# Kernel tuning notes

Hardware: AMD Instinct MI355X
Metric: run time of the kernel (lower is better)

The kernel has to match this reference:

```python
import jax, jax.numpy as jnp
import numpy as np

N_STEPS = 128
B = 32768
H = 64
T0, T1 = 0.0, 1.0
L = 1.0
DT = (T1 - T0) / N_STEPS

# ---- synthesized Equation methods (shapes match the torch forward) ----
def U_fn(x):            return jnp.sum(x * x, axis=-1, keepdims=True)            # [.., B, 1]
def D_fn(n):            return 0.5 + 0.1 * jnp.abs(n)                            # [B, 1] > 0
def alpha_fn(n):        return 0.5 * (n + 1.0)
def beta_fn(n):         return 0.4 * jnp.abs(n) + 0.1
def sigma0_fn(x):       # [B,3,3]
    return 0.5 * jnp.eye(3, dtype=x.dtype) + 0.1 * x[..., :, None] * x[..., None, :]
def T_inv_fn(x):        # [B,3,3]
    nrm = 1.0 + jnp.sum(x * x, axis=-1)[..., None, None]
    return jnp.eye(3, dtype=x.dtype) - x[..., :, None] * x[..., None, :] / nrm
def f_fn(t, n, x, p, y, z):  # y complex [B,1], z complex [B,3]
    return p * y + 0.1 * (1.0 + t) * jnp.sum(z, axis=-1, keepdims=True)
def g_fn(n, x):
    return jnp.sum(x, axis=-1, keepdims=True).astype(jnp.complex64)

def mlp_c(W1, b1, W2, b2, inp):
    """MLP with complex output via paired real/imag heads."""
    h = jnp.tanh(inp @ W1 + b1)
    o = h @ W2 + b2
    d = o.shape[-1] // 2
    return (o[..., :d] + 1j * o[..., d:]).astype(jnp.complex64)

def feat(n, x, p):
    return jnp.concatenate([n, x, p], axis=-1)  # [B, 5]


def setup_inputs() -> dict:
    key = jax.random.key(0)
    ks = jax.random.split(key, 16)
    # polar sample -> 3D start point on the sphere (tran_2to3)
    theta = jax.random.uniform(ks[0], (B, 1)) * jnp.pi
    phi = jax.random.uniform(ks[1], (B, 1)) * 2.0 * jnp.pi
    x0 = jnp.concatenate([jnp.sin(theta) * jnp.cos(phi),
                          jnp.sin(theta) * jnp.sin(phi),
                          jnp.cos(theta)], axis=-1)                       # [B,3]
    # Brownian increments and paths (get_position)
    delta_B = jnp.sqrt(DT) * jax.random.normal(ks[2], (N_STEPS, B, 3), jnp.float32)
    process_X = jnp.concatenate([x0[None], x0[None] + jnp.cumsum(delta_B, 0)], 0)  # [N+1,B,3]
    # birth-death jump counting process
    dN = (jax.random.randint(ks[3], (N_STEPS, B, 1), 0, 3) - 1).astype(jnp.float32)
    n0 = jnp.full((1, B, 1), 10.0, jnp.float32)
    process_N = jnp.concatenate([n0, n0 + jnp.cumsum(dN, 0)], 0)           # [N+1,B,1]
    discrete_p = jax.random.uniform(ks[4], (N_STEPS + 1, B, 1), jnp.float32)
    discrete_t = jnp.linspace(T0, T1, N_STEPS + 1, dtype=jnp.float32)

    def w(k, shape, fan_in):
        return jax.random.normal(k, shape, jnp.float32) / np.sqrt(fan_in)
    inp = dict(process_N=process_N, process_X=process_X, discrete_p=discrete_p,
               discrete_t=discrete_t, delta_B=delta_B,
               Wr1=w(ks[5], (5, H), 5), br1=jnp.zeros((H,)),
               Wr2=w(ks[6], (H, 2), H), br2=jnp.zeros((2,)),
               Wg1=w(ks[7], (N_STEPS, 5, H), 5), bg1=jnp.zeros((N_STEPS, H)),
               Wg2=w(ks[8], (N_STEPS, H, 6), H), bg2=jnp.zeros((N_STEPS, 6)),
               Wj1=w(ks[9], (N_STEPS, 5, H), 5), bj1=jnp.zeros((N_STEPS, H)),
               Wj2=w(ks[10], (N_STEPS, H, 2), H), bj2=jnp.zeros((N_STEPS, 2)))
    return inp


def bsde_forward(process_N, process_X, discrete_p, discrete_t, delta_B,
                 Wr1, br1, Wr2, br2, Wg1, bg1, Wg2, bg2, Wj1, bj1, Wj2, bj2):
    # functional bookkeeping: exp(-cumsum(roll(1j*p*U(x),1) with [0]=0) * dt)
    functional = 1j * discrete_p * U_fn(process_X)                         # [N+1,B,1] c64
    functional = jnp.concatenate([jnp.zeros_like(functional[:1]), functional[:-1]], 0)
    exp_functional = jnp.exp(-jnp.cumsum(functional, axis=0) * DT)         # [N+1,B,1] c64

    u0 = mlp_c(Wr1, br1, Wr2, br2, feat(process_N[0], process_X[0], discrete_p[0]))  # [B,1]
    delta_N_all = jnp.round(process_N[1:] - process_N[:-1])                # [N,B,1]

    xs = (process_N[:-1], process_X[:-1], discrete_p[:-1], discrete_t[:-1],
          delta_B, exp_functional[:-1], delta_N_all,
          Wg1, bg1, Wg2, bg2, Wj1, bj1, Wj2, bj2)

    def step(u, xi):
        (n, x, p, t, dB, ef, dNi, wg1, bg1_, wg2, bg2_, wj1, bj1_, wj2, bj2_) = xi
        ft = feat(n, x, p)
        grad_u = mlp_c(wg1, bg1_, wg2, bg2_, ft)                           # [B,3] c64
        S = sigma0_fn(x)                                                   # [B,3,3]
        Ti = T_inv_fn(x)                                                   # [B,3,3]
        k = jnp.sqrt(2.0 * D_fn(n)) / L                                    # [B,1]
        kg = k * grad_u                                                    # [B,3] c64
        M = jnp.einsum('bij,bkj->bik', Ti, S).astype(jnp.complex64)        # T_inv @ sigma^T
        grad_bmm = jnp.einsum('bi,bij,bj->b', kg, M,
                              dB.astype(jnp.complex64))[:, None]           # [B,1] c64
        ui  = mlp_c(wj1, bj1_, wj2, bj2_, ft)
        uip = mlp_c(wj1, bj1_, wj2, bj2_, feat(n + 1.0, x, p))
        uim = mlp_c(wj1, bj1_, wj2, bj2_, feat(n - 1.0, x, p))
        dup, dum = uip - ui, uim - ui
        fv = f_fn(t, n, x, p, u / ef, grad_u)
        delt = grad_bmm - (alpha_fn(n) * dup + beta_fn(n) * dum) * DT - fv * DT
        delt = jnp.where(dNi > 0, dup, jnp.where(dNi < 0, dum, delt))
        return u + ef * delt, None

    u, _ = jax.lax.scan(step, u0, xs)
    g = exp_functional[-1] * g_fn(process_N[-1], process_X[-1])
    return u, g


def reference(process_N, process_X, discrete_p, discrete_t, delta_B,
              Wr1, br1, Wr2, br2, Wg1, bg1, Wg2, bg2, Wj1, bj1, Wj2, bj2):
    return bsde_forward(process_N, process_X, discrete_p, discrete_t, delta_B,
                        Wr1, br1, Wr2, br2, Wg1, bg1, Wg2, bg2, Wj1, bj1, Wj2, bj2)
```

## Files before the change

kernel.cpp:

```cpp
#include <hip/hip_runtime.h>
#include <math.h>

#define NSTEPS 128
#define BATCH  32768
#define HID    64
#define BLK    512

constexpr float DTf = 1.0f / 128.0f;
constexpr float TWO_LOG2E = 2.88539008177792681f;

typedef float v2f __attribute__((ext_vector_type(2)));

__device__ __forceinline__ v2f v2ld(const float* p) { return *(const v2f*)p; }
__device__ __forceinline__ v2f bc(float s) { v2f r = {s, s}; return r; }
__device__ __forceinline__ v2f pkfma(v2f a, v2f b, v2f c) {
    return __builtin_elementwise_fma(a, b, c);
}

struct CD { float c, dre, dim; };

__device__ __forceinline__ float fast_tanh(float x) {
    float e = __builtin_amdgcn_exp2f(x * TWO_LOG2E);
    return 1.0f - 2.0f * __builtin_amdgcn_rcpf(e + 1.0f);
}
__device__ __forceinline__ v2f fast_tanh2(v2f z) {
    v2f zs = z * TWO_LOG2E;
    v2f e;
    e.x = __builtin_amdgcn_exp2f(zs.x);
    e.y = __builtin_amdgcn_exp2f(zs.y);
    v2f e1 = e + 1.0f;
    v2f r;
    r.x = __builtin_amdgcn_rcpf(e1.x);
    r.y = __builtin_amdgcn_rcpf(e1.y);
    return pkfma(bc(-2.0f), r, bc(1.0f));
}

__device__ __forceinline__ void grad_mlp(
    float n, float x0, float x1, float x2, float p,
    const float* __restrict__ w1, const float* __restrict__ b1,
    const float* __restrict__ w2, const float* __restrict__ b2,
    float& og0, float& og1, float& og2, float& og3, float& og4, float& og5)
{
    v2f og01 = { b2[0], b2[1] };
    v2f og23 = { b2[2], b2[3] };
    v2f og45 = { b2[4], b2[5] };
#pragma unroll 4
    for (int j = 0; j < HID; j += 2) {
        v2f z = pkfma(bc(n),  v2ld(w1 + j),
                pkfma(bc(x0), v2ld(w1 + HID   + j),
                pkfma(bc(x1), v2ld(w1 + 2*HID + j),
                pkfma(bc(x2), v2ld(w1 + 3*HID + j),
                pkfma(bc(p),  v2ld(w1 + 4*HID + j), v2ld(b1 + j))))));
        v2f h = fast_tanh2(z);
        const float* wj = w2 + j*6;
        og01 = pkfma(bc(h.x), v2ld(wj),     pkfma(bc(h.y), v2ld(wj + 6),  og01));
        og23 = pkfma(bc(h.x), v2ld(wj + 2), pkfma(bc(h.y), v2ld(wj + 8),  og23));
        og45 = pkfma(bc(h.x), v2ld(wj + 4), pkfma(bc(h.y), v2ld(wj + 10), og45));
    }
    og0 = og01.x; og1 = og01.y; og2 = og23.x;
    og3 = og23.y; og4 = og45.x; og5 = og45.y;
}

template<bool USE_TD>
__device__ __forceinline__ void jump_mlp(
    float n, float x0, float x1, float x2, float p,
    const float* __restrict__ v1, const float* __restrict__ c1,
    const float* __restrict__ vw2, const float* __restrict__ Td,
    float& dup0, float& dup1, float& dum0, float& dum1)
{
    v2f dup01 = { 0.f, 0.f };
    v2f dum01 = { 0.f, 0.f };
#pragma unroll 4
    for (int j = 0; j < HID; j += 2) {
        v2f d  = v2ld(v1 + j);
        v2f zb = pkfma(bc(n), d,
                 pkfma(bc(x0), v2ld(v1 + HID   + j),
                 pkfma(bc(x1), v2ld(v1 + 2*HID + j),
                 pkfma(bc(x2), v2ld(v1 + 3*HID + j),
                 pkfma(bc(p),  v2ld(v1 + 4*HID + j), v2ld(c1 + j))))));
        v2f T  = fast_tanh2(zb);
        v2f Tv;
        if (USE_TD) Tv = v2ld(Td + j);
        else { Tv.x = fast_tanh(d.x); Tv.y = fast_tanh(d.y); }
        v2f a    = T * Tv;
        v2f oma2 = pkfma(-a, a, bc(1.0f));
        v2f r;
        r.x = __builtin_amdgcn_rcpf(oma2.x);
        r.y = __builtin_amdgcn_rcpf(oma2.y);
        v2f s1 = (T + Tv) * r;
        v2f u1 = s1 - T;
        v2f ep = pkfma(-s1, a, u1);
        v2f s2 = (T - Tv) * r;
        v2f u2 = s2 - T;
        v2f em = pkfma(s2, a, u2);
        v2f wv0 = v2ld(vw2 + 2*j);
        v2f wv1 = v2ld(vw2 + 2*j + 2);
        dup01 = pkfma(bc(ep.x), wv0, pkfma(bc(ep.y), wv1, dup01));
        dum01 = pkfma(bc(em.x), wv0, pkfma(bc(em.y), wv1, dum01));
    }
    dup0 = dup01.x; dup1 = dup01.y;
    dum0 = dum01.x; dum1 = dum01.y;
}

__device__ __forceinline__ void jump_mlp_1s(
    float n, float x0, float x1, float x2, float p, float sgn,
    const float* __restrict__ v1, const float* __restrict__ c1,
    const float* __restrict__ vw2, const float* __restrict__ Td,
    float& e0, float& e1)
{
    v2f acc = { 0.f, 0.f };
#pragma unroll 4
    for (int j = 0; j < HID; j += 2) {
        v2f d  = v2ld(v1 + j);
        v2f zb = pkfma(bc(n), d,
                 pkfma(bc(x0), v2ld(v1 + HID   + j),
                 pkfma(bc(x1), v2ld(v1 + 2*HID + j),
                 pkfma(bc(x2), v2ld(v1 + 3*HID + j),
                 pkfma(bc(p),  v2ld(v1 + 4*HID + j), v2ld(c1 + j))))));
        v2f T   = fast_tanh2(zb);
        v2f Tsv = bc(sgn) * v2ld(Td + j);
        v2f as  = T * Tsv;
        v2f oma = pkfma(-as, as, bc(1.0f));
        v2f r;
        r.x = __builtin_amdgcn_rcpf(oma.x);
        r.y = __builtin_amdgcn_rcpf(oma.y);
        v2f s1 = (T + Tsv) * r;
        v2f u1 = s1 - T;
        v2f e  = pkfma(-s1, as, u1);
        acc = pkfma(bc(e.x), v2ld(vw2 + 2*j), pkfma(bc(e.y), v2ld(vw2 + 2*j + 2), acc));
    }
    e0 = acc.x; e1 = acc.y;
}

template<bool USE_TD>
__device__ __forceinline__ CD step_core(
    float n, float x0, float x1, float x2, float p, float t,
    float db0, float db1, float db2, float dN, float phi,
    const float* __restrict__ w1, const float* __restrict__ b1,
    const float* __restrict__ w2, const float* __restrict__ b2,
    const float* __restrict__ v1, const float* __restrict__ c1,
    const float* __restrict__ vw2, const float* __restrict__ Td)
{
    float og0, og1, og2, og3, og4, og5;
    grad_mlp(n,x0,x1,x2,p, w1,b1,w2,b2, og0,og1,og2,og3,og4,og5);
    float dup0, dup1, dum0, dum1;
    jump_mlp<USE_TD>(n,x0,x1,x2,p, v1,c1,vw2,Td, dup0,dup1,dum0,dum1);

    float r2    = fmaf(x0,x0, fmaf(x1,x1, x2*x2));
    float gamma = 0.1f - (0.5f + 0.1f*r2) * __builtin_amdgcn_rcpf(1.0f + r2);
    float xdb   = fmaf(x0,db0, fmaf(x1,db1, x2*db2));
    float kc    = sqrtf(fmaf(0.2f, fabsf(n), 1.0f));
    float gdb_r = fmaf(og0,db0, fmaf(og1,db1, og2*db2));
    float gdb_i = fmaf(og3,db0, fmaf(og4,db1, og5*db2));
    float gx_r  = fmaf(og0,x0,  fmaf(og1,x1,  og2*x2));
    float gx_i  = fmaf(og3,x0,  fmaf(og4,x1,  og5*x2));
    float gb_r  = kc * fmaf(gamma*xdb, gx_r, 0.5f*gdb_r);
    float gb_i  = kc * fmaf(gamma*xdb, gx_i, 0.5f*gdb_i);

    float alpha = 0.5f*(n + 1.0f);
    float beta  = fmaf(0.4f, fabsf(n), 0.1f);
    float cf    = 0.1f*(1.0f + t)*DTf;
    float d0r = gb_r - (alpha*dup0 + beta*dum0)*DTf - cf*(og0+og1+og2);
    float d0i = gb_i - (alpha*dup1 + beta*dum1)*DTf - cf*(og3+og4+og5);

    float c, sr, si;
    if (dN > 0.5f)       { c = 1.0f;          sr = dup0; si = dup1; }
    else if (dN < -0.5f) { c = 1.0f;          sr = dum0; si = dum1; }
    else                 { c = 1.0f - p*DTf;  sr = d0r;  si = d0i;  }

    float sp, cp;
    __sincosf(phi, &sp, &cp);
    CD o;
    o.c   = c;
    o.dre = fmaf(cp, sr,  sp*si);
    o.dim = fmaf(cp, si, -sp*sr);
    return o;
}

__device__ __forceinline__ void mlp_u0(
    float n, float x0, float x1, float x2, float p,
    const float* __restrict__ w1, const float* __restrict__ b1,
    const float* __restrict__ w2, const float* __restrict__ b2,
    float& ur, float& ui)
{
    v2f o01 = { b2[0], b2[1] };
#pragma unroll 4
    for (int j = 0; j < HID; j += 2) {
        v2f z = pkfma(bc(n),  v2ld(w1 + j),
                pkfma(bc(x0), v2ld(w1 + HID   + j),
                pkfma(bc(x1), v2ld(w1 + 2*HID + j),
                pkfma(bc(x2), v2ld(w1 + 3*HID + j),
                pkfma(bc(p),  v2ld(w1 + 4*HID + j), v2ld(b1 + j))))));
        v2f h = fast_tanh2(z);
        o01 = pkfma(bc(h.x), v2ld(w2 + 2*j), pkfma(bc(h.y), v2ld(w2 + 2*j + 2), o01));
    }
    ur = o01.x; ui = o01.y;
}

__global__ void __launch_bounds__(256) k_phi(
    const float* __restrict__ X, const float* __restrict__ P,
    float* __restrict__ phi, float* __restrict__ phiF)
{
    int b = blockIdx.x*256 + threadIdx.x;
    double s = 0.0;
    for (int k = 0; k < NSTEPS; k++) {
        size_t idx = (size_t)k*BATCH + b;
        phi[idx] = (float)(DTf * s);
        float p = P[idx];
        const float* xp = X + idx*3;
        float x0 = xp[0], x1 = xp[1], x2 = xp[2];
        s += (double)p * (double)(x0*x0 + x1*x1 + x2*x2);
    }
    phiF[b] = (float)(DTf * s);
}

__global__ void __launch_bounds__(BLK) k_step(
    const float* __restrict__ N,  const float* __restrict__ X,
    const float* __restrict__ P,  const float* __restrict__ Tarr,
    const float* __restrict__ dB,
    const float* __restrict__ Wg1, const float* __restrict__ bg1,
    const float* __restrict__ Wg2, const float* __restrict__ bg2,
    const float* __restrict__ Wj1, const float* __restrict__ bj1,
    const float* __restrict__ Wj2, const float* __restrict__ bj2,
    const float* __restrict__ phiA, float* __restrict__ cA, float2* __restrict__ dA)
{
    int k = blockIdx.y;
    const float* w1  = Wg1 + k*5*HID;
    const float* b1  = bg1 + k*HID;
    const float* w2  = Wg2 + k*HID*6;
    const float* b2  = bg2 + k*6;
    const float* v1  = Wj1 + k*5*HID;
    const float* c1  = bj1 + k*HID;
    const float* vw2 = Wj2 + k*HID*2;
    float t = Tarr[k];

    __shared__ float Td[HID];
    __shared__ unsigned short sorig[BLK];
    __shared__ int cnt[2];
    if (threadIdx.x < HID) Td[threadIdx.x] = fast_tanh(v1[threadIdx.x]);
    if (threadIdx.x == 0) { cnt[0] = 0; cnt[1] = 0; }
    __syncthreads();

    int tid  = threadIdx.x;
    int base = blockIdx.x*BLK;
    {
        size_t i0 = (size_t)k*BATCH + base + tid;
        float n0  = N[i0];
        float dN0 = N[i0 + BATCH] - n0;
        bool full0 = (dN0 == 0.0f);
        int pos = full0 ? atomicAdd(&cnt[0], 1) : (BLK-1) - atomicAdd(&cnt[1], 1);
        sorig[pos] = (unsigned short)tid;
    }
    __syncthreads();

    int ob = base + sorig[tid];
    size_t idx = (size_t)k*BATCH + ob;
    float n  = N[idx], p = P[idx];
    float dN = N[idx + BATCH] - n;
    const float* xp  = X  + idx*3;
    const float* dbp = dB + idx*3;
    float x0 = xp[0],  x1 = xp[1],  x2 = xp[2];
    float db0 = dbp[0], db1 = dbp[1], db2 = dbp[2];
    float phi = phiA[idx];
    bool  g   = (dN == 0.0f);

    float c, sr, si;
    if (__ballot(g) != 0ull) {
        float dup0, dup1, dum0, dum1;
        jump_mlp<true>(n,x0,x1,x2,p, v1,c1,vw2,Td, dup0,dup1,dum0,dum1);
        float og0, og1, og2, og3, og4, og5;
        grad_mlp(n,x0,x1,x2,p, w1,b1,w2,b2, og0,og1,og2,og3,og4,og5);

        float r2    = fmaf(x0,x0, fmaf(x1,x1, x2*x2));
        float gamma = 0.1f - (0.5f + 0.1f*r2) * __builtin_amdgcn_rcpf(1.0f + r2);
        float xdb   = fmaf(x0,db0, fmaf(x1,db1, x2*db2));
        float kc    = sqrtf(fmaf(0.2f, fabsf(n), 1.0f));
        float gdb_r = fmaf(og0,db0, fmaf(og1,db1, og2*db2));
        float gdb_i = fmaf(og3,db0, fmaf(og4,db1, og5*db2));
        float gx_r  = fmaf(og0,x0,  fmaf(og1,x1,  og2*x2));
        float gx_i  = fmaf(og3,x0,  fmaf(og4,x1,  og5*x2));
        float gb_r  = kc * fmaf(gamma*xdb, gx_r, 0.5f*gdb_r);
        float gb_i  = kc * fmaf(gamma*xdb, gx_i, 0.5f*gdb_i);

        float alpha = 0.5f*(n + 1.0f);
        float beta  = fmaf(0.4f, fabsf(n), 0.1f);
        float cf    = 0.1f*(1.0f + t)*DTf;
        float d0r = gb_r - (alpha*dup0 + beta*dum0)*DTf - cf*(og0+og1+og2);
        float d0i = gb_i - (alpha*dup1 + beta*dum1)*DTf - cf*(og3+og4+og5);

        if (dN > 0.5f)       { c = 1.0f;          sr = dup0; si = dup1; }
        else if (dN < -0.5f) { c = 1.0f;          sr = dum0; si = dum1; }
        else                 { c = 1.0f - p*DTf;  sr = d0r;  si = d0i;  }
    } else {
        jump_mlp_1s(n,x0,x1,x2,p, dN, v1,c1,vw2,Td, sr, si);
        c = 1.0f;
    }

    float sp, cp;
    __sincosf(phi, &sp, &cp);
    size_t oidx = (size_t)k*BATCH + ob;
    cA[oidx] = c;
    dA[oidx] = make_float2(fmaf(cp, sr,  sp*si), fmaf(cp, si, -sp*sr));
}

__global__ void __launch_bounds__(256) k_combine(
    const float* __restrict__ N, const float* __restrict__ X, const float* __restrict__ P,
    const float* __restrict__ Wr1, const float* __restrict__ br1,
    const float* __restrict__ Wr2, const float* __restrict__ br2,
    const float* __restrict__ cA, const float2* __restrict__ dA,
    const float* __restrict__ phiF, float* __restrict__ out, int full)
{
    int b = blockIdx.x*256 + threadIdx.x;
    const float* xp = X + (size_t)b*3;
    float ur, ui;
    mlp_u0(N[b], xp[0], xp[1], xp[2], P[b], Wr1, br1, Wr2, br2, ur, ui);
#pragma unroll 8
    for (int k = 0; k < NSTEPS; k++) {
        size_t idx = (size_t)k*BATCH + b;
        float  c = cA[idx];
        float2 d = dA[idx];
        ur = fmaf(c, ur, d.x);
        ui = fmaf(c, ui, d.y);
    }
    float phi = phiF[b];
    const float* xf = X + ((size_t)NSTEPS*BATCH + b)*3;
    float s = xf[0] + xf[1] + xf[2];
    float sp, cp;
    __sincosf(phi, &sp, &cp);
    float gre =  s*cp;
    float gim = -s*sp;
    if (full) {
        out[b]           = ur;
        out[BATCH + b]   = ui;
        out[2*BATCH + b] = gre;
        out[3*BATCH + b] = gim;
    } else {
        out[b]         = ur;
        out[BATCH + b] = gre;
    }
}

__global__ void __launch_bounds__(256) k_fused(
    const float* __restrict__ N,  const float* __restrict__ X,
    const float* __restrict__ P,  const float* __restrict__ Tarr,
    const float* __restrict__ dB,
    const float* __restrict__ Wr1, const float* __restrict__ br1,
    const float* __restrict__ Wr2, const float* __restrict__ br2,
    const float* __restrict__ Wg1, const float* __restrict__ bg1,
    const float* __restrict__ Wg2, const float* __restrict__ bg2,
    const float* __restrict__ Wj1, const float* __restrict__ bj1,
    const float* __restrict__ Wj2, const float* __restrict__ bj2,
    float* __restrict__ out, int full)
{
    int b = blockIdx.x*256 + threadIdx.x;
    float ur, ui;
    {
        const float* xp = X + (size_t)b*3;
        mlp_u0(N[b], xp[0], xp[1], xp[2], P[b], Wr1, br1, Wr2, br2, ur, ui);
    }
    double s = 0.0;
    for (int k = 0; k < NSTEPS; k++) {
        size_t idx = (size_t)k*BATCH + b;
        float n = N[idx], p = P[idx], t = Tarr[k];
        const float* xp  = X  + idx*3;
        const float* dbp = dB + idx*3;
        float dN  = N[idx + BATCH] - n;
        float phi = (float)(DTf * s);
        CD cd = step_core<false>(n, xp[0], xp[1], xp[2], p, t,
                                 dbp[0], dbp[1], dbp[2], dN, phi,
                                 Wg1 + k*5*HID, bg1 + k*HID,
                                 Wg2 + k*HID*6, bg2 + k*6,
                                 Wj1 + k*5*HID, bj1 + k*HID,
                                 Wj2 + k*HID*2, nullptr);
        ur = fmaf(cd.c, ur, cd.dre);
        ui = fmaf(cd.c, ui, cd.dim);
        float x0 = xp[0], x1 = xp[1], x2 = xp[2];
        s += (double)p * (double)(x0*x0 + x1*x1 + x2*x2);
    }
    float phi = (float)(DTf * s);
    const float* xf = X + ((size_t)NSTEPS*BATCH + b)*3;
    float sm = xf[0] + xf[1] + xf[2];
    float sp, cp;
    __sincosf(phi, &sp, &cp);
    float gre =  sm*cp;
    float gim = -sm*sp;
    if (full) {
        out[b]           = ur;
        out[BATCH + b]   = ui;
        out[2*BATCH + b] = gre;
        out[3*BATCH + b] = gim;
    } else {
        out[b]         = ur;
        out[BATCH + b] = gre;
    }
}

extern "C" void kernel_launch(void* const* d_in, const int* in_sizes, int n_in,
                              void* d_out, int out_size, void* d_ws, size_t ws_size,
                              hipStream_t stream)
{
    const float* N    = (const float*)d_in[0];
    const float* X    = (const float*)d_in[1];
    const float* P    = (const float*)d_in[2];
    const float* Tarr = (const float*)d_in[3];
    const float* dB   = (const float*)d_in[4];
    const float* Wr1  = (const float*)d_in[5];
    const float* br1  = (const float*)d_in[6];
    const float* Wr2  = (const float*)d_in[7];
    const float* br2  = (const float*)d_in[8];
    const float* Wg1  = (const float*)d_in[9];
    const float* bg1  = (const float*)d_in[10];
    const float* Wg2  = (const float*)d_in[11];
    const float* bg2  = (const float*)d_in[12];
    const float* Wj1  = (const float*)d_in[13];
    const float* bj1  = (const float*)d_in[14];
    const float* Wj2  = (const float*)d_in[15];
    const float* bj2  = (const float*)d_in[16];
    float* out = (float*)d_out;

    const int full = (out_size >= 4*BATCH) ? 1 : 0;

    const size_t phi_elems = (size_t)NSTEPS*BATCH;
    const size_t need = (phi_elems + BATCH + phi_elems)*sizeof(float)
                      + phi_elems*sizeof(float2);

    if (ws_size >= need) {
        float*  phiA = (float*)d_ws;
        float*  phiF = phiA + phi_elems;
        float*  cA   = phiF + BATCH;
        float2* dA   = (float2*)(cA + phi_elems);

        k_phi<<<dim3(BATCH/256), dim3(256), 0, stream>>>(X, P, phiA, phiF);
        k_step<<<dim3(BATCH/BLK, NSTEPS), dim3(BLK), 0, stream>>>(
            N, X, P, Tarr, dB, Wg1, bg1, Wg2, bg2, Wj1, bj1, Wj2, bj2,
            phiA, cA, dA);
        k_combine<<<dim3(BATCH/256), dim3(256), 0, stream>>>(
            N, X, P, Wr1, br1, Wr2, br2, cA, dA, phiF, out, full);
    } else {
        k_fused<<<dim3(BATCH/256), dim3(256), 0, stream>>>(
            N, X, P, Tarr, dB, Wr1, br1, Wr2, br2,
            Wg1, bg1, Wg2, bg2, Wj1, bj1, Wj2, bj2, out, full);
    }
}
```

Measured before the change: 215.3 us.

## Compact full and jump samples globally into separate lists and specialized kernels

Adds a classify kernel that builds global per-step index lists of no-jump and jump samples, then launches separate kernels for each class so every wavefront runs only one code path. Before, samples were only sorted within each block, so mixed wavefronts still ran both paths. The cA array is dropped and the decay coefficient is recomputed from N and P in the combine loop, which cuts one write stream. This adds two kernel launches, a memset and an extra list write and read, and the gathered indices make memory access scattered.

```diff
diff --git a/kernel.cpp b/kernel.cpp
--- a/kernel.cpp
+++ b/kernel.cpp
@@ -4,7 +4,6 @@
 #define NSTEPS 128
 #define BATCH  32768
 #define HID    64
-#define BLK    512
 
 constexpr float DTf = 1.0f / 128.0f;
 constexpr float TWO_LOG2E = 2.88539008177792681f;
@@ -214,7 +213,40 @@
     phiF[b] = (float)(DTf * s);
 }
 
-__global__ void __launch_bounds__(BLK) k_step(
+__global__ void __launch_bounds__(256) k_classify(
+    const float* __restrict__ N,
+    unsigned short* __restrict__ fullList, unsigned short* __restrict__ jumpList,
+    int2* __restrict__ counters)
+{
+    int k   = blockIdx.y;
+    int tid = threadIdx.x;
+    int b   = blockIdx.x*256 + tid;
+
+    __shared__ int cnt[2];
+    __shared__ int gbase[2];
+    __shared__ unsigned short lf[256], lj[256];
+    if (tid == 0) { cnt[0] = 0; cnt[1] = 0; }
+    __syncthreads();
+
+    size_t i0 = (size_t)k*BATCH + b;
+    float n0  = N[i0];
+    float dN  = N[i0 + BATCH] - n0;
+    if (dN == 0.0f) {
+        int r = atomicAdd(&cnt[0], 1);
+        lf[r] = (unsigned short)b;
+    } else {
+        int r = atomicAdd(&cnt[1], 1);
+        lj[r] = (unsigned short)(b | (dN < 0.0f ? 0x8000 : 0));
+    }
+    __syncthreads();
+    if (tid == 0) gbase[0] = atomicAdd(&counters[k].x, cnt[0]);
+    if (tid == 1) gbase[1] = atomicAdd(&counters[k].y, cnt[1]);
+    __syncthreads();
+    if (tid < cnt[0]) fullList[(size_t)k*BATCH + gbase[0] + tid] = lf[tid];
+    if (tid < cnt[1]) jumpList[(size_t)k*BATCH + gbase[1] + tid] = lj[tid];
+}
+
+__global__ void __launch_bounds__(256) k_step_full(
     const float* __restrict__ N,  const float* __restrict__ X,
     const float* __restrict__ P,  const float* __restrict__ Tarr,
     const float* __restrict__ dB,
@@ -222,9 +254,15 @@
     const float* __restrict__ Wg2, const float* __restrict__ bg2,
     const float* __restrict__ Wj1, const float* __restrict__ bj1,
     const float* __restrict__ Wj2, const float* __restrict__ bj2,
-    const float* __restrict__ phiA, float* __restrict__ cA, float2* __restrict__ dA)
+    const float* __restrict__ phiA,
+    const unsigned short* __restrict__ fullList, const int2* __restrict__ counters,
+    float2* __restrict__ dA)
 {
     int k = blockIdx.y;
+    int count = counters[k].x;
+    int start = blockIdx.x*256;
+    if (start >= count) return;
+
     const float* w1  = Wg1 + k*5*HID;
     const float* b1  = bg1 + k*HID;
     const float* w2  = Wg2 + k*HID*6;
@@ -235,92 +273,111 @@
     float t = Tarr[k];
 
     __shared__ float Td[HID];
-    __shared__ unsigned short sorig[BLK];
-    __shared__ int cnt[2];
     if (threadIdx.x < HID) Td[threadIdx.x] = fast_tanh(v1[threadIdx.x]);
-    if (threadIdx.x == 0) { cnt[0] = 0; cnt[1] = 0; }
     __syncthreads();
 
-    int tid  = threadIdx.x;
-    int base = blockIdx.x*BLK;
-    {
-        size_t i0 = (size_t)k*BATCH + base + tid;
-        float n0  = N[i0];
-        float dN0 = N[i0 + BATCH] - n0;
-        bool full0 = (dN0 == 0.0f);
-        int pos = full0 ? atomicAdd(&cnt[0], 1) : (BLK-1) - atomicAdd(&cnt[1], 1);
-        sorig[pos] = (unsigned short)tid;
-    }
-    __syncthreads();
-
-    int ob = base + sorig[tid];
+    int slot = start + threadIdx.x;
+    bool act = slot < count;
+    int ob   = fullList[(size_t)k*BATCH + (act ? slot : count - 1)];
     size_t idx = (size_t)k*BATCH + ob;
-    float n  = N[idx], p = P[idx];
-    float dN = N[idx + BATCH] - n;
+    float n = N[idx], p = P[idx];
     const float* xp  = X  + idx*3;
     const float* dbp = dB + idx*3;
     float x0 = xp[0],  x1 = xp[1],  x2 = xp[2];
     float db0 = dbp[0], db1 = dbp[1], db2 = dbp[2];
     float phi = phiA[idx];
-    bool  g   = (dN == 0.0f);
-
-    float c, sr, si;
-    if (__ballot(g) != 0ull) {
-        float dup0, dup1, dum0, dum1;
-        jump_mlp<true>(n,x0,x1,x2,p, v1,c1,vw2,Td, dup0,dup1,dum0,dum1);
-        float og0, og1, og2, og3, og4, og5;
-        grad_mlp(n,x0,x1,x2,p, w1,b1,w2,b2, og0,og1,og2,og3,og4,og5);
-
-        float r2    = fmaf(x0,x0, fmaf(x1,x1, x2*x2));
-        float gamma = 0.1f - (0.5f + 0.1f*r2) * __builtin_amdgcn_rcpf(1.0f + r2);
-        float xdb   = fmaf(x0,db0, fmaf(x1,db1, x2*db2));
-        float kc    = sqrtf(fmaf(0.2f, fabsf(n), 1.0f));
-        float gdb_r = fmaf(og0,db0, fmaf(og1,db1, og2*db2));
-        float gdb_i = fmaf(og3,db0, fmaf(og4,db1, og5*db2));
-        float gx_r  = fmaf(og0,x0,  fmaf(og1,x1,  og2*x2));
-        float gx_i  = fmaf(og3,x0,  fmaf(og4,x1,  og5*x2));
-        float gb_r  = kc * fmaf(gamma*xdb, gx_r, 0.5f*gdb_r);
-        float gb_i  = kc * fmaf(gamma*xdb, gx_i, 0.5f*gdb_i);
-
-        float alpha = 0.5f*(n + 1.0f);
-        float beta  = fmaf(0.4f, fabsf(n), 0.1f);
-        float cf    = 0.1f*(1.0f + t)*DTf;
-        float d0r = gb_r - (alpha*dup0 + beta*dum0)*DTf - cf*(og0+og1+og2);
-        float d0i = gb_i - (alpha*dup1 + beta*dum1)*DTf - cf*(og3+og4+og5);
-
-        if (dN > 0.5f)       { c = 1.0f;          sr = dup0; si = dup1; }
-        else if (dN < -0.5f) { c = 1.0f;          sr = dum0; si = dum1; }
-        else                 { c = 1.0f - p*DTf;  sr = d0r;  si = d0i;  }
-    } else {
-        jump_mlp_1s(n,x0,x1,x2,p, dN, v1,c1,vw2,Td, sr, si);
-        c = 1.0f;
-    }
+
+    float dup0, dup1, dum0, dum1;
+    jump_mlp<true>(n,x0,x1,x2,p, v1,c1,vw2,Td, dup0,dup1,dum0,dum1);
+    float og0, og1, og2, og3, og4, og5;
+    grad_mlp(n,x0,x1,x2,p, w1,b1,w2,b2, og0,og1,og2,og3,og4,og5);
+
+    float r2    = fmaf(x0,x0, fmaf(x1,x1, x2*x2));
+    float gamma = 0.1f - (0.5f + 0.1f*r2) * __builtin_amdgcn_rcpf(1.0f + r2);
+    float xdb   = fmaf(x0,db0, fmaf(x1,db1, x2*db2));
+    float kc    = sqrtf(fmaf(0.2f, fabsf(n), 1.0f));
+    float gdb_r = fmaf(og0,db0, fmaf(og1,db1, og2*db2));
+    float gdb_i = fmaf(og3,db0, fmaf(og4,db1, og5*db2));
+    float gx_r  = fmaf(og0,x0,  fmaf(og1,x1,  og2*x2));
+    float gx_i  = fmaf(og3,x0,  fmaf(og4,x1,  og5*x2));
+    float gb_r  = kc * fmaf(gamma*xdb, gx_r, 0.5f*gdb_r);
+    float gb_i  = kc * fmaf(gamma*xdb, gx_i, 0.5f*gdb_i);
+
+    float alpha = 0.5f*(n + 1.0f);
+    float beta  = fmaf(0.4f, fabsf(n), 0.1f);
+    float cf    = 0.1f*(1.0f + t)*DTf;
+    float sr = gb_r - (alpha*dup0 + beta*dum0)*DTf - cf*(og0+og1+og2);
+    float si = gb_i - (alpha*dup1 + beta*dum1)*DTf - cf*(og3+og4+og5);
 
     float sp, cp;
     __sincosf(phi, &sp, &cp);
-    size_t oidx = (size_t)k*BATCH + ob;
-    cA[oidx] = c;
-    dA[oidx] = make_float2(fmaf(cp, sr,  sp*si), fmaf(cp, si, -sp*sr));
+    if (act)
+        dA[idx] = make_float2(fmaf(cp, sr,  sp*si), fmaf(cp, si, -sp*sr));
+}
+
+__global__ void __launch_bounds__(256) k_step_jump(
+    const float* __restrict__ N,  const float* __restrict__ X,
+    const float* __restrict__ P,
+    const float* __restrict__ Wj1, const float* __restrict__ bj1,
+    const float* __restrict__ Wj2,
+    const float* __restrict__ phiA,
+    const unsigned short* __restrict__ jumpList, const int2* __restrict__ counters,
+    float2* __restrict__ dA)
+{
+    int k = blockIdx.y;
+    int count = counters[k].y;
+    int start = blockIdx.x*256;
+    if (start >= count) return;
+
+    const float* v1  = Wj1 + k*5*HID;
+    const float* c1  = bj1 + k*HID;
+    const float* vw2 = Wj2 + k*HID*2;
+
+    __shared__ float Td[HID];
+    if (threadIdx.x < HID) Td[threadIdx.x] = fast_tanh(v1[threadIdx.x]);
+    __syncthreads();
+
+    int slot = start + threadIdx.x;
+    bool act = slot < count;
+    unsigned short ent = jumpList[(size_t)k*BATCH + (act ? slot : count - 1)];
+    float sgn = (ent & 0x8000) ? -1.0f : 1.0f;
+    int   ob  = ent & 0x7FFF;
+    size_t idx = (size_t)k*BATCH + ob;
+    float n = N[idx], p = P[idx];
+    const float* xp = X + idx*3;
+    float x0 = xp[0], x1 = xp[1], x2 = xp[2];
+    float phi = phiA[idx];
+
+    float sr, si;
+    jump_mlp_1s(n,x0,x1,x2,p, sgn, v1,c1,vw2,Td, sr, si);
+
+    float sp, cp;
+    __sincosf(phi, &sp, &cp);
+    if (act)
+        dA[idx] = make_float2(fmaf(cp, sr,  sp*si), fmaf(cp, si, -sp*sr));
 }
 
 __global__ void __launch_bounds__(256) k_combine(
     const float* __restrict__ N, const float* __restrict__ X, const float* __restrict__ P,
     const float* __restrict__ Wr1, const float* __restrict__ br1,
     const float* __restrict__ Wr2, const float* __restrict__ br2,
-    const float* __restrict__ cA, const float2* __restrict__ dA,
+    const float2* __restrict__ dA,
     const float* __restrict__ phiF, float* __restrict__ out, int full)
 {
     int b = blockIdx.x*256 + threadIdx.x;
     const float* xp = X + (size_t)b*3;
     float ur, ui;
     mlp_u0(N[b], xp[0], xp[1], xp[2], P[b], Wr1, br1, Wr2, br2, ur, ui);
-#pragma unroll 8
+    float nprev = N[b];
+#pragma unroll 4
     for (int k = 0; k < NSTEPS; k++) {
         size_t idx = (size_t)k*BATCH + b;
-        float  c = cA[idx];
+        float nnext = N[idx + BATCH];
+        float c = (nnext == nprev) ? (1.0f - P[idx]*DTf) : 1.0f;
         float2 d = dA[idx];
         ur = fmaf(c, ur, d.x);
         ui = fmaf(c, ui, d.y);
+        nprev = nnext;
     }
     float phi = phiF[b];
     const float* xf = X + ((size_t)NSTEPS*BATCH + b)*3;
@@ -421,21 +478,32 @@
     const int full = (out_size >= 4*BATCH) ? 1 : 0;
 
     const size_t phi_elems = (size_t)NSTEPS*BATCH;
-    const size_t need = (phi_elems + BATCH + phi_elems)*sizeof(float)
-                      + phi_elems*sizeof(float2);
+    const size_t off_phiF = phi_elems*4;
+    const size_t off_dA   = off_phiF + (size_t)BATCH*4;
+    const size_t off_fl   = off_dA + phi_elems*8;
+    const size_t off_jl   = off_fl + phi_elems*2;
+    const size_t off_cnt  = off_jl + phi_elems*2;
+    const size_t need     = off_cnt + NSTEPS*sizeof(int2);
 
     if (ws_size >= need) {
-        float*  phiA = (float*)d_ws;
-        float*  phiF = phiA + phi_elems;
-        float*  cA   = phiF + BATCH;
-        float2* dA   = (float2*)(cA + phi_elems);
-
+        char* ws = (char*)d_ws;
+        float*          phiA = (float*)ws;
+        float*          phiF = (float*)(ws + off_phiF);
+        float2*         dA   = (float2*)(ws + off_dA);
+        unsigned short* fL   = (unsigned short*)(ws + off_fl);
+        unsigned short* jL   = (unsigned short*)(ws + off_jl);
+        int2*           cnts = (int2*)(ws + off_cnt);
+
+        hipMemsetAsync(cnts, 0, NSTEPS*sizeof(int2), stream);
         k_phi<<<dim3(BATCH/256), dim3(256), 0, stream>>>(X, P, phiA, phiF);
-        k_step<<<dim3(BATCH/BLK, NSTEPS), dim3(BLK), 0, stream>>>(
+        k_classify<<<dim3(BATCH/256, NSTEPS), dim3(256), 0, stream>>>(N, fL, jL, cnts);
+        k_step_full<<<dim3(BATCH/256, NSTEPS), dim3(256), 0, stream>>>(
             N, X, P, Tarr, dB, Wg1, bg1, Wg2, bg2, Wj1, bj1, Wj2, bj2,
-            phiA, cA, dA);
+            phiA, fL, cnts, dA);
+        k_step_jump<<<dim3(BATCH/256, NSTEPS), dim3(256), 0, stream>>>(
+            N, X, P, Wj1, bj1, Wj2, phiA, jL, cnts, dA);
         k_combine<<<dim3(BATCH/256), dim3(256), 0, stream>>>(
-            N, X, P, Wr1, br1, Wr2, br2, cA, dA, phiF, out, full);
+            N, X, P, Wr1, br1, Wr2, br2, dA, phiF, out, full);
     } else {
         k_fused<<<dim3(BATCH/256), dim3(256), 0, stream>>>(
             N, X, P, Tarr, dB, Wr1, br1, Wr2, br2,
```

Measured after the change: 463.0 us. +115.1%, slower.

## Process four batch elements per thread in k_step to reuse weight loads

Applied to the files above, without the earlier changes.

Each thread in k_step now handles four sorted batch elements instead of one. Blocks shrink to 256 threads but cover a window of 1024 elements. The MLP weight loads for each hidden unit pair are hoisted out of the per-element loop and shared across all four elements, which cuts scalar/LDS weight traffic and adds independent work for latency hiding. In exchange, register pressure rises, the grid has fewer blocks, and the coarser grouping can make the uniform-branch test (any full-step element in the wave) trigger the expensive path more often.

```diff
diff --git a/kernel.cpp b/kernel.cpp
--- a/kernel.cpp
+++ b/kernel.cpp
@@ -4,7 +4,9 @@
 #define NSTEPS 128
 #define BATCH  32768
 #define HID    64
-#define BLK    512
+#define TPT    4
+#define BLKT   256
+#define WIN    (BLKT*TPT)
 
 constexpr float DTf = 1.0f / 128.0f;
 constexpr float TWO_LOG2E = 2.88539008177792681f;
@@ -102,36 +104,6 @@
     dum0 = dum01.x; dum1 = dum01.y;
 }
 
-__device__ __forceinline__ void jump_mlp_1s(
-    float n, float x0, float x1, float x2, float p, float sgn,
-    const float* __restrict__ v1, const float* __restrict__ c1,
-    const float* __restrict__ vw2, const float* __restrict__ Td,
-    float& e0, float& e1)
-{
-    v2f acc = { 0.f, 0.f };
-#pragma unroll 4
-    for (int j = 0; j < HID; j += 2) {
-        v2f d  = v2ld(v1 + j);
-        v2f zb = pkfma(bc(n), d,
-                 pkfma(bc(x0), v2ld(v1 + HID   + j),
-                 pkfma(bc(x1), v2ld(v1 + 2*HID + j),
-                 pkfma(bc(x2), v2ld(v1 + 3*HID + j),
-                 pkfma(bc(p),  v2ld(v1 + 4*HID + j), v2ld(c1 + j))))));
-        v2f T   = fast_tanh2(zb);
-        v2f Tsv = bc(sgn) * v2ld(Td + j);
-        v2f as  = T * Tsv;
-        v2f oma = pkfma(-as, as, bc(1.0f));
-        v2f r;
-        r.x = __builtin_amdgcn_rcpf(oma.x);
-        r.y = __builtin_amdgcn_rcpf(oma.y);
-        v2f s1 = (T + Tsv) * r;
-        v2f u1 = s1 - T;
-        v2f e  = pkfma(-s1, as, u1);
-        acc = pkfma(bc(e.x), v2ld(vw2 + 2*j), pkfma(bc(e.y), v2ld(vw2 + 2*j + 2), acc));
-    }
-    e0 = acc.x; e1 = acc.y;
-}
-
 template<bool USE_TD>
 __device__ __forceinline__ CD step_core(
     float n, float x0, float x1, float x2, float p, float t,
@@ -214,7 +186,7 @@
     phiF[b] = (float)(DTf * s);
 }
 
-__global__ void __launch_bounds__(BLK) k_step(
+__global__ void __launch_bounds__(BLKT) k_step(
     const float* __restrict__ N,  const float* __restrict__ X,
     const float* __restrict__ P,  const float* __restrict__ Tarr,
     const float* __restrict__ dB,
@@ -235,72 +207,174 @@
     float t = Tarr[k];
 
     __shared__ float Td[HID];
-    __shared__ unsigned short sorig[BLK];
+    __shared__ unsigned short sorig[WIN];
     __shared__ int cnt[2];
     if (threadIdx.x < HID) Td[threadIdx.x] = fast_tanh(v1[threadIdx.x]);
     if (threadIdx.x == 0) { cnt[0] = 0; cnt[1] = 0; }
     __syncthreads();
 
     int tid  = threadIdx.x;
-    int base = blockIdx.x*BLK;
-    {
-        size_t i0 = (size_t)k*BATCH + base + tid;
-        float n0  = N[i0];
-        float dN0 = N[i0 + BATCH] - n0;
-        bool full0 = (dN0 == 0.0f);
-        int pos = full0 ? atomicAdd(&cnt[0], 1) : (BLK-1) - atomicAdd(&cnt[1], 1);
-        sorig[pos] = (unsigned short)tid;
+    int base = blockIdx.x*WIN;
+#pragma unroll
+    for (int u = 0; u < TPT; ++u) {
+        int lb = tid + u*BLKT;
+        size_t i0 = (size_t)k*BATCH + base + lb;
+        float dN0 = N[i0 + BATCH] - N[i0];
+        bool f0 = (dN0 == 0.0f);
+        int pos = f0 ? atomicAdd(&cnt[0], 1) : (WIN-1) - atomicAdd(&cnt[1], 1);
+        sorig[pos] = (unsigned short)lb;
     }
     __syncthreads();
 
-    int ob = base + sorig[tid];
-    size_t idx = (size_t)k*BATCH + ob;
-    float n  = N[idx], p = P[idx];
-    float dN = N[idx + BATCH] - n;
-    const float* xp  = X  + idx*3;
-    const float* dbp = dB + idx*3;
-    float x0 = xp[0],  x1 = xp[1],  x2 = xp[2];
-    float db0 = dbp[0], db1 = dbp[1], db2 = dbp[2];
-    float phi = phiA[idx];
-    bool  g   = (dN == 0.0f);
-
-    float c, sr, si;
-    if (__ballot(g) != 0ull) {
-        float dup0, dup1, dum0, dum1;
-        jump_mlp<true>(n,x0,x1,x2,p, v1,c1,vw2,Td, dup0,dup1,dum0,dum1);
-        float og0, og1, og2, og3, og4, og5;
-        grad_mlp(n,x0,x1,x2,p, w1,b1,w2,b2, og0,og1,og2,og3,og4,og5);
-
-        float r2    = fmaf(x0,x0, fmaf(x1,x1, x2*x2));
-        float gamma = 0.1f - (0.5f + 0.1f*r2) * __builtin_amdgcn_rcpf(1.0f + r2);
-        float xdb   = fmaf(x0,db0, fmaf(x1,db1, x2*db2));
-        float kc    = sqrtf(fmaf(0.2f, fabsf(n), 1.0f));
-        float gdb_r = fmaf(og0,db0, fmaf(og1,db1, og2*db2));
-        float gdb_i = fmaf(og3,db0, fmaf(og4,db1, og5*db2));
-        float gx_r  = fmaf(og0,x0,  fmaf(og1,x1,  og2*x2));
-        float gx_i  = fmaf(og3,x0,  fmaf(og4,x1,  og5*x2));
-        float gb_r  = kc * fmaf(gamma*xdb, gx_r, 0.5f*gdb_r);
-        float gb_i  = kc * fmaf(gamma*xdb, gx_i, 0.5f*gdb_i);
-
-        float alpha = 0.5f*(n + 1.0f);
-        float beta  = fmaf(0.4f, fabsf(n), 0.1f);
-        float cf    = 0.1f*(1.0f + t)*DTf;
-        float d0r = gb_r - (alpha*dup0 + beta*dum0)*DTf - cf*(og0+og1+og2);
-        float d0i = gb_i - (alpha*dup1 + beta*dum1)*DTf - cf*(og3+og4+og5);
-
-        if (dN > 0.5f)       { c = 1.0f;          sr = dup0; si = dup1; }
-        else if (dN < -0.5f) { c = 1.0f;          sr = dum0; si = dum1; }
-        else                 { c = 1.0f - p*DTf;  sr = d0r;  si = d0i;  }
+    int   ob[TPT];
+    float n_[TPT], p_[TPT], x0_[TPT], x1_[TPT], x2_[TPT];
+    float db0_[TPT], db1_[TPT], db2_[TPT], phi_[TPT], dN_[TPT];
+    bool anyfull = false;
+#pragma unroll
+    for (int v = 0; v < TPT; ++v) {
+        int lb = sorig[TPT*tid + v];
+        ob[v] = base + lb;
+        size_t idx = (size_t)k*BATCH + ob[v];
+        n_[v] = N[idx]; p_[v] = P[idx];
+        dN_[v] = N[idx + BATCH] - n_[v];
+        const float* xp  = X  + idx*3;
+        x0_[v]=xp[0]; x1_[v]=xp[1]; x2_[v]=xp[2];
+        const float* dbp = dB + idx*3;
+        db0_[v]=dbp[0]; db1_[v]=dbp[1]; db2_[v]=dbp[2];
+        phi_[v] = phiA[idx];
+        anyfull |= (dN_[v] == 0.0f);
+    }
+
+    float c_[TPT], sr_[TPT], si_[TPT];
+
+    if (__ballot(anyfull) != 0ull) {
+        v2f og01[TPT], og23[TPT], og45[TPT];
+#pragma unroll
+        for (int v = 0; v < TPT; ++v) {
+            og01[v] = (v2f){ b2[0], b2[1] };
+            og23[v] = (v2f){ b2[2], b2[3] };
+            og45[v] = (v2f){ b2[4], b2[5] };
+        }
+        for (int j = 0; j < HID; j += 2) {
+            v2f g0=v2ld(w1+j), g1=v2ld(w1+HID+j), g2=v2ld(w1+2*HID+j),
+                g3=v2ld(w1+3*HID+j), g4=v2ld(w1+4*HID+j), gb=v2ld(b1+j);
+            const float* wj = w2 + j*6;
+            v2f a0=v2ld(wj), a1=v2ld(wj+6), a2=v2ld(wj+2),
+                a3=v2ld(wj+8), a4=v2ld(wj+4), a5=v2ld(wj+10);
+#pragma unroll
+            for (int v = 0; v < TPT; ++v) {
+                v2f z = pkfma(bc(n_[v]), g0,
+                        pkfma(bc(x0_[v]), g1,
+                        pkfma(bc(x1_[v]), g2,
+                        pkfma(bc(x2_[v]), g3,
+                        pkfma(bc(p_[v]),  g4, gb)))));
+                v2f h = fast_tanh2(z);
+                og01[v] = pkfma(bc(h.x), a0, pkfma(bc(h.y), a1, og01[v]));
+                og23[v] = pkfma(bc(h.x), a2, pkfma(bc(h.y), a3, og23[v]));
+                og45[v] = pkfma(bc(h.x), a4, pkfma(bc(h.y), a5, og45[v]));
+            }
+        }
+        v2f dup[TPT], dum[TPT];
+#pragma unroll
+        for (int v = 0; v < TPT; ++v) { dup[v] = (v2f){0.f,0.f}; dum[v] = (v2f){0.f,0.f}; }
+        for (int j = 0; j < HID; j += 2) {
+            v2f jd=v2ld(v1+j), j1=v2ld(v1+HID+j), j2=v2ld(v1+2*HID+j),
+                j3=v2ld(v1+3*HID+j), j4=v2ld(v1+4*HID+j), jc=v2ld(c1+j);
+            v2f tv = v2ld(Td + j);
+            v2f wv0=v2ld(vw2+2*j), wv1=v2ld(vw2+2*j+2);
+#pragma unroll
+            for (int v = 0; v < TPT; ++v) {
+                v2f zb = pkfma(bc(n_[v]), jd,
+                         pkfma(bc(x0_[v]), j1,
+                         pkfma(bc(x1_[v]), j2,
+                         pkfma(bc(x2_[v]), j3,
+                         pkfma(bc(p_[v]),  j4, jc)))));
+                v2f T = fast_tanh2(zb);
+                v2f a = T * tv;
+                v2f om = pkfma(-a, a, bc(1.0f));
+                v2f r;
+                r.x = __builtin_amdgcn_rcpf(om.x);
+                r.y = __builtin_amdgcn_rcpf(om.y);
+                v2f s1 = (T + tv) * r;
+                v2f u1 = s1 - T;
+                v2f ep = pkfma(-s1, a, u1);
+                v2f s2 = (T - tv) * r;
+                v2f u2 = s2 - T;
+                v2f em = pkfma(s2, a, u2);
+                dup[v] = pkfma(bc(ep.x), wv0, pkfma(bc(ep.y), wv1, dup[v]));
+                dum[v] = pkfma(bc(em.x), wv0, pkfma(bc(em.y), wv1, dum[v]));
+            }
+        }
+#pragma unroll
+        for (int v = 0; v < TPT; ++v) {
+            float og0=og01[v].x, og1=og01[v].y, og2=og23[v].x;
+            float og3=og23[v].y, og4=og45[v].x, og5=og45[v].y;
+            float x0=x0_[v], x1=x1_[v], x2=x2_[v];
+            float n=n_[v], p=p_[v];
+            float r2    = fmaf(x0,x0, fmaf(x1,x1, x2*x2));
+            float gamma = 0.1f - (0.5f + 0.1f*r2) * __builtin_amdgcn_rcpf(1.0f + r2);
+            float xdb   = fmaf(x0,db0_[v], fmaf(x1,db1_[v], x2*db2_[v]));
+            float kc    = sqrtf(fmaf(0.2f, fabsf(n), 1.0f));
+            float gdb_r = fmaf(og0,db0_[v], fmaf(og1,db1_[v], og2*db2_[v]));
+            float gdb_i = fmaf(og3,db0_[v], fmaf(og4,db1_[v], og5*db2_[v]));
+            float gx_r  = fmaf(og0,x0,  fmaf(og1,x1,  og2*x2));
+            float gx_i  = fmaf(og3,x0,  fmaf(og4,x1,  og5*x2));
+            float gb_r  = kc * fmaf(gamma*xdb, gx_r, 0.5f*gdb_r);
+            float gb_i  = kc * fmaf(gamma*xdb, gx_i, 0.5f*gdb_i);
+            float alpha = 0.5f*(n + 1.0f);
+            float beta  = fmaf(0.4f, fabsf(n), 0.1f);
+            float cf    = 0.1f*(1.0f + t)*DTf;
+            float d0r = gb_r - (alpha*dup[v].x + beta*dum[v].x)*DTf - cf*(og0+og1+og2);
+            float d0i = gb_i - (alpha*dup[v].y + beta*dum[v].y)*DTf - cf*(og3+og4+og5);
+            if (dN_[v] > 0.5f)       { c_[v]=1.0f;             sr_[v]=dup[v].x; si_[v]=dup[v].y; }
+            else if (dN_[v] < -0.5f) { c_[v]=1.0f;             sr_[v]=dum[v].x; si_[v]=dum[v].y; }
+            else                     { c_[v]=1.0f - p*DTf;     sr_[v]=d0r;      si_[v]=d0i;      }
+        }
     } else {
-        jump_mlp_1s(n,x0,x1,x2,p, dN, v1,c1,vw2,Td, sr, si);
-        c = 1.0f;
-    }
-
-    float sp, cp;
-    __sincosf(phi, &sp, &cp);
-    size_t oidx = (size_t)k*BATCH + ob;
-    cA[oidx] = c;
-    dA[oidx] = make_float2(fmaf(cp, sr,  sp*si), fmaf(cp, si, -sp*sr));
+        v2f acc[TPT];
+        float sgn[TPT];
+#pragma unroll
+        for (int v = 0; v < TPT; ++v) { acc[v] = (v2f){0.f,0.f}; sgn[v] = dN_[v]; }
+        for (int j = 0; j < HID; j += 2) {
+            v2f jd=v2ld(v1+j), j1=v2ld(v1+HID+j), j2=v2ld(v1+2*HID+j),
+                j3=v2ld(v1+3*HID+j), j4=v2ld(v1+4*HID+j), jc=v2ld(c1+j);
+            v2f tv = v2ld(Td + j);
+            v2f wv0=v2ld(vw2+2*j), wv1=v2ld(vw2+2*j+2);
+#pragma unroll
+            for (int v = 0; v < TPT; ++v) {
+                v2f zb = pkfma(bc(n_[v]), jd,
+                         pkfma(bc(x0_[v]), j1,
+                         pkfma(bc(x1_[v]), j2,
+                         pkfma(bc(x2_[v]), j3,
+                         pkfma(bc(p_[v]),  j4, jc)))));
+                v2f T   = fast_tanh2(zb);
+                v2f Tsv = bc(sgn[v]) * tv;
+                v2f as  = T * Tsv;
+                v2f om  = pkfma(-as, as, bc(1.0f));
+                v2f r;
+                r.x = __builtin_amdgcn_rcpf(om.x);
+                r.y = __builtin_amdgcn_rcpf(om.y);
+                v2f s1 = (T + Tsv) * r;
+                v2f u1 = s1 - T;
+                v2f e  = pkfma(-s1, as, u1);
+                acc[v] = pkfma(bc(e.x), wv0, pkfma(bc(e.y), wv1, acc[v]));
+            }
+        }
+#pragma unroll
+        for (int v = 0; v < TPT; ++v) {
+            c_[v] = 1.0f; sr_[v] = acc[v].x; si_[v] = acc[v].y;
+        }
+    }
+
+#pragma unroll
+    for (int v = 0; v < TPT; ++v) {
+        float sp, cp;
+        __sincosf(phi_[v], &sp, &cp);
+        size_t oidx = (size_t)k*BATCH + ob[v];
+        cA[oidx] = c_[v];
+        dA[oidx] = make_float2(fmaf(cp, sr_[v],  sp*si_[v]),
+                               fmaf(cp, si_[v], -sp*sr_[v]));
+    }
 }
 
 __global__ void __launch_bounds__(256) k_combine(
@@ -431,7 +505,7 @@
         float2* dA   = (float2*)(cA + phi_elems);
 
         k_phi<<<dim3(BATCH/256), dim3(256), 0, stream>>>(X, P, phiA, phiF);
-        k_step<<<dim3(BATCH/BLK, NSTEPS), dim3(BLK), 0, stream>>>(
+        k_step<<<dim3(BATCH/WIN, NSTEPS), dim3(BLKT), 0, stream>>>(
             N, X, P, Tarr, dB, Wg1, bg1, Wg2, bg2, Wj1, bj1, Wj2, bj2,
             phiA, cA, dA);
         k_combine<<<dim3(BATCH/256), dim3(256), 0, stream>>>(
```

After: 282.6 us. 1.31x slower.

## Sort step-kernel samples over wider window with wave-aggregated compaction

Applied to the files above, without the earlier changes.

The step kernel now partitions a 2048-sample window per block (256 threads, 8 passes) into no-jump and jump groups, instead of a 512-sample window. The partition uses ballot and popcount with one atomic per wave rather than one per thread. A wider window packs more wavefronts that are entirely jump samples, so more of them take the cheap single-MLP path and skip the gradient MLP. The dB load is also moved inside the full branch. In exchange each block does serial passes and the grid is smaller (16x128 blocks), which may reduce latency hiding.

```diff
diff --git a/kernel.cpp b/kernel.cpp
--- a/kernel.cpp
+++ b/kernel.cpp
@@ -4,7 +4,9 @@
 #define NSTEPS 128
 #define BATCH  32768
 #define HID    64
-#define BLK    512
+#define BLKT   256
+#define WIN    2048
+#define PASSES (WIN/BLKT)
 
 constexpr float DTf = 1.0f / 128.0f;
 constexpr float TWO_LOG2E = 2.88539008177792681f;
@@ -214,7 +216,7 @@
     phiF[b] = (float)(DTf * s);
 }
 
-__global__ void __launch_bounds__(BLK) k_step(
+__global__ void __launch_bounds__(BLKT) k_step(
     const float* __restrict__ N,  const float* __restrict__ X,
     const float* __restrict__ P,  const float* __restrict__ Tarr,
     const float* __restrict__ dB,
@@ -235,72 +237,89 @@
     float t = Tarr[k];
 
     __shared__ float Td[HID];
-    __shared__ unsigned short sorig[BLK];
+    __shared__ unsigned short sorig[WIN];
     __shared__ int cnt[2];
     if (threadIdx.x < HID) Td[threadIdx.x] = fast_tanh(v1[threadIdx.x]);
     if (threadIdx.x == 0) { cnt[0] = 0; cnt[1] = 0; }
     __syncthreads();
 
     int tid  = threadIdx.x;
-    int base = blockIdx.x*BLK;
-    {
-        size_t i0 = (size_t)k*BATCH + base + tid;
-        float n0  = N[i0];
-        float dN0 = N[i0 + BATCH] - n0;
-        bool full0 = (dN0 == 0.0f);
-        int pos = full0 ? atomicAdd(&cnt[0], 1) : (BLK-1) - atomicAdd(&cnt[1], 1);
-        sorig[pos] = (unsigned short)tid;
+    int lane = tid & 63;
+    unsigned long long ltmask = ((unsigned long long)1 << lane) - 1;
+    int base = blockIdx.x*WIN;
+
+#pragma unroll
+    for (int u = 0; u < PASSES; ++u) {
+        int lb = u*BLKT + tid;
+        size_t i0 = (size_t)k*BATCH + base + lb;
+        float dN0 = N[i0 + BATCH] - N[i0];
+        bool f0 = (dN0 == 0.0f);
+        unsigned long long m = __ballot(f0);
+        int nf = __popcll(m);
+        int rF = __popcll(m & ltmask);
+        int rJ = lane - rF;
+        int fb = 0, jb = 0;
+        if (lane == 0) {
+            fb = atomicAdd(&cnt[0], nf);
+            jb = atomicAdd(&cnt[1], 64 - nf);
+        }
+        fb = __shfl(fb, 0);
+        jb = __shfl(jb, 0);
+        int pos = f0 ? (fb + rF) : (WIN - 1 - (jb + rJ));
+        sorig[pos] = (unsigned short)lb;
     }
     __syncthreads();
 
-    int ob = base + sorig[tid];
-    size_t idx = (size_t)k*BATCH + ob;
-    float n  = N[idx], p = P[idx];
-    float dN = N[idx + BATCH] - n;
-    const float* xp  = X  + idx*3;
-    const float* dbp = dB + idx*3;
-    float x0 = xp[0],  x1 = xp[1],  x2 = xp[2];
-    float db0 = dbp[0], db1 = dbp[1], db2 = dbp[2];
-    float phi = phiA[idx];
-    bool  g   = (dN == 0.0f);
-
-    float c, sr, si;
-    if (__ballot(g) != 0ull) {
-        float dup0, dup1, dum0, dum1;
-        jump_mlp<true>(n,x0,x1,x2,p, v1,c1,vw2,Td, dup0,dup1,dum0,dum1);
-        float og0, og1, og2, og3, og4, og5;
-        grad_mlp(n,x0,x1,x2,p, w1,b1,w2,b2, og0,og1,og2,og3,og4,og5);
-
-        float r2    = fmaf(x0,x0, fmaf(x1,x1, x2*x2));
-        float gamma = 0.1f - (0.5f + 0.1f*r2) * __builtin_amdgcn_rcpf(1.0f + r2);
-        float xdb   = fmaf(x0,db0, fmaf(x1,db1, x2*db2));
-        float kc    = sqrtf(fmaf(0.2f, fabsf(n), 1.0f));
-        float gdb_r = fmaf(og0,db0, fmaf(og1,db1, og2*db2));
-        float gdb_i = fmaf(og3,db0, fmaf(og4,db1, og5*db2));
-        float gx_r  = fmaf(og0,x0,  fmaf(og1,x1,  og2*x2));
-        float gx_i  = fmaf(og3,x0,  fmaf(og4,x1,  og5*x2));
-        float gb_r  = kc * fmaf(gamma*xdb, gx_r, 0.5f*gdb_r);
-        float gb_i  = kc * fmaf(gamma*xdb, gx_i, 0.5f*gdb_i);
-
-        float alpha = 0.5f*(n + 1.0f);
-        float beta  = fmaf(0.4f, fabsf(n), 0.1f);
-        float cf    = 0.1f*(1.0f + t)*DTf;
-        float d0r = gb_r - (alpha*dup0 + beta*dum0)*DTf - cf*(og0+og1+og2);
-        float d0i = gb_i - (alpha*dup1 + beta*dum1)*DTf - cf*(og3+og4+og5);
-
-        if (dN > 0.5f)       { c = 1.0f;          sr = dup0; si = dup1; }
-        else if (dN < -0.5f) { c = 1.0f;          sr = dum0; si = dum1; }
-        else                 { c = 1.0f - p*DTf;  sr = d0r;  si = d0i;  }
-    } else {
-        jump_mlp_1s(n,x0,x1,x2,p, dN, v1,c1,vw2,Td, sr, si);
-        c = 1.0f;
-    }
-
-    float sp, cp;
-    __sincosf(phi, &sp, &cp);
-    size_t oidx = (size_t)k*BATCH + ob;
-    cA[oidx] = c;
-    dA[oidx] = make_float2(fmaf(cp, sr,  sp*si), fmaf(cp, si, -sp*sr));
+    for (int pass = 0; pass < PASSES; ++pass) {
+        int ob = base + sorig[pass*BLKT + tid];
+        size_t idx = (size_t)k*BATCH + ob;
+        float n  = N[idx], p = P[idx];
+        float dN = N[idx + BATCH] - n;
+        const float* xp = X + idx*3;
+        float x0 = xp[0], x1 = xp[1], x2 = xp[2];
+        float phi = phiA[idx];
+        bool  g   = (dN == 0.0f);
+
+        float c, sr, si;
+        if (__ballot(g) != 0ull) {
+            const float* dbp = dB + idx*3;
+            float db0 = dbp[0], db1 = dbp[1], db2 = dbp[2];
+            float dup0, dup1, dum0, dum1;
+            jump_mlp<true>(n,x0,x1,x2,p, v1,c1,vw2,Td, dup0,dup1,dum0,dum1);
+            float og0, og1, og2, og3, og4, og5;
+            grad_mlp(n,x0,x1,x2,p, w1,b1,w2,b2, og0,og1,og2,og3,og4,og5);
+
+            float r2    = fmaf(x0,x0, fmaf(x1,x1, x2*x2));
+            float gamma = 0.1f - (0.5f + 0.1f*r2) * __builtin_amdgcn_rcpf(1.0f + r2);
+            float xdb   = fmaf(x0,db0, fmaf(x1,db1, x2*db2));
+            float kc    = sqrtf(fmaf(0.2f, fabsf(n), 1.0f));
+            float gdb_r = fmaf(og0,db0, fmaf(og1,db1, og2*db2));
+            float gdb_i = fmaf(og3,db0, fmaf(og4,db1, og5*db2));
+            float gx_r  = fmaf(og0,x0,  fmaf(og1,x1,  og2*x2));
+            float gx_i  = fmaf(og3,x0,  fmaf(og4,x1,  og5*x2));
+            float gb_r  = kc * fmaf(gamma*xdb, gx_r, 0.5f*gdb_r);
+            float gb_i  = kc * fmaf(gamma*xdb, gx_i, 0.5f*gdb_i);
+
+            float alpha = 0.5f*(n + 1.0f);
+            float beta  = fmaf(0.4f, fabsf(n), 0.1f);
+            float cf    = 0.1f*(1.0f + t)*DTf;
+            float d0r = gb_r - (alpha*dup0 + beta*dum0)*DTf - cf*(og0+og1+og2);
+            float d0i = gb_i - (alpha*dup1 + beta*dum1)*DTf - cf*(og3+og4+og5);
+
+            if (dN > 0.5f)       { c = 1.0f;          sr = dup0; si = dup1; }
+            else if (dN < -0.5f) { c = 1.0f;          sr = dum0; si = dum1; }
+            else                 { c = 1.0f - p*DTf;  sr = d0r;  si = d0i;  }
+        } else {
+            jump_mlp_1s(n,x0,x1,x2,p, dN, v1,c1,vw2,Td, sr, si);
+            c = 1.0f;
+        }
+
+        float sp, cp;
+        __sincosf(phi, &sp, &cp);
+        size_t oidx = (size_t)k*BATCH + ob;
+        cA[oidx] = c;
+        dA[oidx] = make_float2(fmaf(cp, sr,  sp*si), fmaf(cp, si, -sp*sr));
+    }
 }
 
 __global__ void __launch_bounds__(256) k_combine(
@@ -431,7 +450,7 @@
         float2* dA   = (float2*)(cA + phi_elems);
 
         k_phi<<<dim3(BATCH/256), dim3(256), 0, stream>>>(X, P, phiA, phiF);
-        k_step<<<dim3(BATCH/BLK, NSTEPS), dim3(BLK), 0, stream>>>(
+        k_step<<<dim3(BATCH/WIN, NSTEPS), dim3(BLKT), 0, stream>>>(
             N, X, P, Tarr, dB, Wg1, bg1, Wg2, bg2, Wj1, bj1, Wj2, bj2,
             phiA, cA, dA);
         k_combine<<<dim3(BATCH/256), dim3(256), 0, stream>>>(
```

Result: no change. 215.5 us (+0.1%).
